# Kernel tuning notes

Measured on AMD Instinct MI355X. Metric: run time of the kernel, lower is better.

## Reference

```python
import jax, jax.numpy as jnp
import numpy as np

FS = 160        # frame shift (samples per frame)
MU = 255.0      # mu-law constant for 256 levels
EMPH = 0.97     # de-emphasis coefficient


def _conv_tanh(x, w, b):
    # Conv1dKeepLength (non-causal, same-length) + tanh. x: (B,L,Cin), w: (K,Cin,Cout)
    K = w.shape[0]
    pad_le = (K - 1) // 2
    pad_ri = (K - 1) - pad_le
    xp = jnp.pad(x, ((0, 0), (pad_le, pad_ri), (0, 0)))
    L = x.shape[1]
    y = b
    for k in range(K):  # tiny fixed kernel loop (K=3)
        y = y + xp[:, k:k + L, :] @ w[k]
    return jnp.tanh(y)


def _forward(features, conv1_w, conv1_b, conv2_w, conv2_b,
             fr_fc1_w, fr_fc1_b, fr_fc2_w, fr_fc2_b,
             gru_wi, gru_wh, gru_bi, gru_bh, out_w, out_b):
    # ---- FrameRateNet: conv-tanh x2 + MLP -> conditioning (B,F,128) ----
    c = _conv_tanh(features, conv1_w, conv1_b)
    c = _conv_tanh(c, conv2_w, conv2_b)
    c = jnp.tanh(c @ fr_fc1_w + fr_fc1_b)
    cond = jnp.tanh(c @ fr_fc2_w + fr_fc2_b)
    # upsample frame-rate conditioning to sample rate: (B, T=F*FS, 128)
    cond_up = jnp.repeat(cond, FS, axis=1)
    B, T, _ = cond_up.shape
    H = gru_wh.shape[1]
    dt = features.dtype

    def step(carry, cond_t):
        h, prev = carry                       # h:(B,H)  prev:(B,1) last emitted sample
        x = jnp.concatenate([prev, cond_t], axis=-1)   # (B, 1+128)
        gi = x @ gru_wi.T + gru_bi            # (B, 3H)
        gh = h @ gru_wh.T + gru_bh
        i_r, i_z, i_n = jnp.split(gi, 3, axis=-1)
        h_r, h_z, h_n = jnp.split(gh, 3, axis=-1)
        r = jax.nn.sigmoid(i_r + h_r)
        z = jax.nn.sigmoid(i_z + h_z)
        n = jnp.tanh(i_n + r * h_n)
        h_new = (1.0 - z) * n + z * h
        logits = h_new @ out_w + out_b        # (B, 256) mu-law categorical logits
        idx = jnp.argmax(logits, axis=-1)     # greedy sampling (deterministic baseline)
        v = (idx.astype(dt) + 0.5) / 128.0 - 1.0           # (-1,1)
        sample = jnp.sign(v) * (jnp.power(1.0 + MU, jnp.abs(v)) - 1.0) / MU
        return (h_new, sample[:, None]), (logits, sample)

    cond_seq = jnp.swapaxes(cond_up, 0, 1)    # (T,B,128)
    init = (jnp.zeros((B, H), dt), jnp.zeros((B, 1), dt))
    _, (logits, samples) = jax.lax.scan(step, init, cond_seq)
    logits = jnp.swapaxes(logits, 0, 1)       # (B,T,256)
    samples = jnp.swapaxes(samples, 0, 1)     # (B,T)

    # ---- de-emphasis IIR: y[t] = s[t] + 0.97*y[t-1] ----
    def de_step(y_prev, s_t):
        y = s_t + EMPH * y_prev
        return y, y
    _, wav = jax.lax.scan(de_step, jnp.zeros((B,), dt), samples.T)
    wav = wav.T[..., None]                    # (B,T,1)
    return wav, logits


def setup_inputs() -> dict:
    key = jax.random.key(0)
    ks = jax.random.split(key, 16)
    B, F, D = 8, 64, 20
    s = 0.05
    return {
        "features": jax.random.normal(ks[0], (B, F, D), jnp.float32),
        "conv1_w": jax.random.normal(ks[1], (3, D, 128), jnp.float32) * s,
        "conv1_b": jnp.zeros((128,), jnp.float32),
        "conv2_w": jax.random.normal(ks[2], (3, 128, 128), jnp.float32) * s,
        "conv2_b": jnp.zeros((128,), jnp.float32),
        "fr_fc1_w": jax.random.normal(ks[3], (128, 128), jnp.float32) * s,
        "fr_fc1_b": jnp.zeros((128,), jnp.float32),
        "fr_fc2_w": jax.random.normal(ks[4], (128, 128), jnp.float32) * s,
        "fr_fc2_b": jnp.zeros((128,), jnp.float32),
        "gru_wi": jax.random.normal(ks[5], (768, 129), jnp.float32) * s,
        "gru_wh": jax.random.normal(ks[6], (768, 256), jnp.float32) * s,
        "gru_bi": jnp.zeros((768,), jnp.float32),
        "gru_bh": jnp.zeros((768,), jnp.float32),
        "out_w": jax.random.normal(ks[7], (256, 256), jnp.float32) * s,
        "out_b": jnp.zeros((256,), jnp.float32),
    }


def reference(features, conv1_w, conv1_b, conv2_w, conv2_b,
              fr_fc1_w, fr_fc1_b, fr_fc2_w, fr_fc2_b,
              gru_wi, gru_wh, gru_bi, gru_bh, out_w, out_b):
    return _forward(features, conv1_w, conv1_b, conv2_w, conv2_b,
                    fr_fc1_w, fr_fc1_b, fr_fc2_w, fr_fc2_b,
                    gru_wi, gru_wh, gru_bi, gru_bh, out_w, out_b)
```

## Files before the change

### kernel.cpp

```cpp
#include <hip/hip_runtime.h>
#include <cmath>


#define NB 8
#define NF 64
#define ND 20
#define NH 256
#define NG 768
#define FS 160
#define NT (NF * FS)
#define NSLOT 768

#define AGENT __HIP_MEMORY_SCOPE_AGENT
#define HLAY(c) ((((c) >> 4) * 20) + ((c) & 15))

typedef float v2f __attribute__((ext_vector_type(2)));

#define PKFMA(acc, w, h) \
    asm("v_pk_fma_f32 %0, %1, %2, %0" : "+v"(acc) : "v"(w), "v"(h))
#define PKFMA_BLO(acc, w, h) \
    asm("v_pk_fma_f32 %0, %1, %2, %0 op_sel:[0,0,0] op_sel_hi:[1,0,1]" \
        : "+v"(acc) : "v"(w), "v"(h))
#define PKFMA_BHI(acc, w, h) \
    asm("v_pk_fma_f32 %0, %1, %2, %0 op_sel:[0,1,0] op_sel_hi:[1,1,1]" \
        : "+v"(acc) : "v"(w), "v"(h))

#define DPP0(x, ctrl) \
    __int_as_float(__builtin_amdgcn_update_dpp( \
        0, __float_as_int(x), (ctrl), 0xf, 0xf, true))
#define DPPOLD(x, ctrl, oldv) \
    __int_as_float(__builtin_amdgcn_update_dpp( \
        __float_as_int(oldv), __float_as_int(x), (ctrl), 0xf, 0xf, false))

static __device__ __forceinline__ float fexp2(float x) {
    float r; asm("v_exp_f32 %0, %1" : "=v"(r) : "v"(x)); return r;
}
static __device__ __forceinline__ float frcp(float x) {
    float r; asm("v_rcp_f32 %0, %1" : "=v"(r) : "v"(x)); return r;
}
#define LOG2E  1.4426950408889634f
#define LOG2E2 2.8853900817779268f
static __device__ __forceinline__ float fsigmoid(float x) {
    return frcp(1.f + fexp2(-x * LOG2E));
}
static __device__ __forceinline__ float ftanh(float x) {
    return 1.f - 2.f * frcp(fexp2(x * LOG2E2) + 1.f);
}

#define BAR() do { \
    __builtin_amdgcn_sched_barrier(0); \
    asm volatile("s_waitcnt lgkmcnt(0)" ::: "memory"); \
    __builtin_amdgcn_s_barrier(); \
    __builtin_amdgcn_sched_barrier(0); } while (0)

__global__ __launch_bounds__(128) void frn_kernel(
    const float* __restrict__ feat,
    const float* __restrict__ w1,
    const float* __restrict__ b1,
    const float* __restrict__ w2,
    const float* __restrict__ b2,
    const float* __restrict__ fw1,
    const float* __restrict__ fb1,
    const float* __restrict__ fw2,
    const float* __restrict__ fb2,
    const float* __restrict__ wi,
    const float* __restrict__ bi,
    float* __restrict__ gic)
{
    const int bf = blockIdx.x;
    const int b = bf >> 6;
    const int f = bf & 63;
    const int o = threadIdx.x;

    __shared__ float sfeat[5][ND];
    __shared__ float sc1[3][128];
    __shared__ float sc2[128];
    __shared__ float sc3[128];
    __shared__ float scond[128];

    for (int i = o; i < 5 * ND; i += 128) {
        int ff = f - 2 + i / ND;
        int c = i % ND;
        sfeat[i / ND][c] = (ff >= 0 && ff < NF) ? feat[((size_t)b * NF + ff) * ND + c] : 0.f;
    }
    __syncthreads();

    for (int df = 0; df < 3; ++df) {
        int fp = f - 1 + df;
        if (fp >= 0 && fp < NF) {
            float acc = b1[o];
            for (int k = 0; k < 3; ++k)
                for (int c = 0; c < ND; ++c)
                    acc += sfeat[df + k][c] * w1[(k * ND + c) * 128 + o];
            sc1[df][o] = tanhf(acc);
        } else {
            sc1[df][o] = 0.f;
        }
    }
    __syncthreads();

    {
        float acc = b2[o];
        for (int k = 0; k < 3; ++k)
            for (int c = 0; c < 128; ++c)
                acc += sc1[k][c] * w2[(k * 128 + c) * 128 + o];
        sc2[o] = tanhf(acc);
    }
    __syncthreads();
    {
        float acc = fb1[o];
        for (int c = 0; c < 128; ++c) acc += sc2[c] * fw1[c * 128 + o];
        sc3[o] = tanhf(acc);
    }
    __syncthreads();
    {
        float acc = fb2[o];
        for (int c = 0; c < 128; ++c) acc += sc3[c] * fw2[c * 128 + o];
        scond[o] = tanhf(acc);
    }
    __syncthreads();

    for (int r = 0; r < 6; ++r) {
        int j = o + 128 * r;
        float acc = bi[j];
        const float* wr = wi + (size_t)j * 129 + 1;
        for (int c = 0; c < 128; ++c) acc += scond[c] * wr[c];
        gic[(size_t)bf * NG + j] = acc;
    }
}

__global__ __launch_bounds__(512, 2) void ar_kernel(
    const float* __restrict__ gic,
    const float* __restrict__ wh,
    const float* __restrict__ ow,
    const float* __restrict__ wi,
    const float* __restrict__ bh,
    const float* __restrict__ ob,
    float* __restrict__ wav_out,
    float* __restrict__ logits_out,
    unsigned long long* __restrict__ hxp)
{
    const int bid = blockIdx.x;
    const int b = bid & 7;
    const int j = bid >> 3;
    const int t = threadIdx.x;
    const int qq = t >> 4;
    const int ss = t & 15;
    const int og = t >> 3;
    const int c8 = t & 7;

    __shared__ __align__(16) float hsp[16 * 20];
    __shared__ __align__(16) float pl[8][260];
    __shared__ float sgi[NG];
    __shared__ float candv[4];
    __shared__ int   candi[4];

    v2f WH0[8], WH1[8], WH2[8];
    {
        const v2f* wb2 = (const v2f*)wh;
        size_t q0 = (size_t)(32 * j + qq) * 128 + ss * 8;
        #pragma unroll
        for (int i = 0; i < 8; ++i) {
            WH0[i] = wb2[q0 + i];
            WH1[i] = wb2[q0 + 256 * 128 + i];
            WH2[i] = wb2[q0 + 512 * 128 + i];
        }
    }
    v2f OWa[32], OWb[32];
    {
        const v2f* op2 = (const v2f*)ow;
        #pragma unroll
        for (int i = 0; i < 32; ++i) {
            OWa[i] = op2[(size_t)(c8 * 32 + i) * 128 + og * 2];
            OWb[i] = op2[(size_t)(c8 * 32 + i) * 128 + og * 2 + 1];
        }
    }

    float bh_r = 0, bh_z = 0, bh_n = 0, wi_r = 0, wi_z = 0, wi_n = 0, ob_o = 0;
    if (t < NH) {
        bh_r = bh[t]; bh_z = bh[t + 256]; bh_n = bh[t + 512];
        wi_r = wi[(size_t)t * 129];
        wi_z = wi[(size_t)(t + 256) * 129];
        wi_n = wi[(size_t)(t + 512) * 129];
        ob_o = ob[t];
        hsp[HLAY(t)] = 0.f;
    }
    float prev = 0.f, yacc = 0.f;
    __syncthreads();

    const float* gf = gic + (size_t)b * NF * NG;
    float* lob = logits_out + (size_t)b * NT * NH;
    float* wob = wav_out + (size_t)b * NT;
    unsigned long long* hxb = hxp + (size_t)b * 2 * NSLOT;
    int fcnt = 0;

    for (int st = 0; st <= NT; ++st) {
        if (st < NT && fcnt == 0) {
            for (int i = t; i < NG; i += 512) sgi[i] = gf[i];
        }

        {
            const float4* h4 = (const float4*)hsp;
            float4 ha0 = h4[ss * 5 + 0];
            float4 ha1 = h4[ss * 5 + 1];
            float4 ha2 = h4[ss * 5 + 2];
            float4 ha3 = h4[ss * 5 + 3];
            float4 hb0 = h4[(c8 * 2) * 5 + 0];
            float4 hb1 = h4[(c8 * 2) * 5 + 1];
            float4 hb2 = h4[(c8 * 2) * 5 + 2];
            float4 hb3 = h4[(c8 * 2) * 5 + 3];
            float4 hb4 = h4[(c8 * 2 + 1) * 5 + 0];
            float4 hb5 = h4[(c8 * 2 + 1) * 5 + 1];
            float4 hb6 = h4[(c8 * 2 + 1) * 5 + 2];
            float4 hb7 = h4[(c8 * 2 + 1) * 5 + 3];

            v2f s0 = {0.f, 0.f}, s1 = {0.f, 0.f}, s2 = {0.f, 0.f};
            {
                v2f lo, hi;
                lo.x = ha0.x; lo.y = ha0.y; hi.x = ha0.z; hi.y = ha0.w;
                PKFMA(s0, WH0[0], lo); PKFMA(s0, WH0[1], hi);
                PKFMA(s1, WH1[0], lo); PKFMA(s1, WH1[1], hi);
                PKFMA(s2, WH2[0], lo); PKFMA(s2, WH2[1], hi);
                lo.x = ha1.x; lo.y = ha1.y; hi.x = ha1.z; hi.y = ha1.w;
                PKFMA(s0, WH0[2], lo); PKFMA(s0, WH0[3], hi);
                PKFMA(s1, WH1[2], lo); PKFMA(s1, WH1[3], hi);
                PKFMA(s2, WH2[2], lo); PKFMA(s2, WH2[3], hi);
                lo.x = ha2.x; lo.y = ha2.y; hi.x = ha2.z; hi.y = ha2.w;
                PKFMA(s0, WH0[4], lo); PKFMA(s0, WH0[5], hi);
                PKFMA(s1, WH1[4], lo); PKFMA(s1, WH1[5], hi);
                PKFMA(s2, WH2[4], lo); PKFMA(s2, WH2[5], hi);
                lo.x = ha3.x; lo.y = ha3.y; hi.x = ha3.z; hi.y = ha3.w;
                PKFMA(s0, WH0[6], lo); PKFMA(s0, WH0[7], hi);
                PKFMA(s1, WH1[6], lo); PKFMA(s1, WH1[7], hi);
                PKFMA(s2, WH2[6], lo); PKFMA(s2, WH2[7], hi);
            }
            float a0 = s0.x + s0.y, a1 = s1.x + s1.y, a2 = s2.x + s2.y;
            a0 += DPP0(a0, 0x111); a1 += DPP0(a1, 0x111); a2 += DPP0(a2, 0x111);
            a0 += DPP0(a0, 0x112); a1 += DPP0(a1, 0x112); a2 += DPP0(a2, 0x112);
            a0 += DPP0(a0, 0x114); a1 += DPP0(a1, 0x114); a2 += DPP0(a2, 0x114);
            a0 += DPP0(a0, 0x118); a1 += DPP0(a1, 0x118); a2 += DPP0(a2, 0x118);
            if (st < NT && ss == 15) {
                unsigned long long tg = (unsigned long long)(unsigned)(st + 1) << 32;
                size_t base = (size_t)(st & 1) * NSLOT + 32 * j + qq;
                (void)__hip_atomic_exchange(&hxb[base],
                    tg | (unsigned long long)__float_as_uint(a0),
                    __ATOMIC_RELAXED, AGENT);
                (void)__hip_atomic_exchange(&hxb[base + 256],
                    tg | (unsigned long long)__float_as_uint(a1),
                    __ATOMIC_RELAXED, AGENT);
                (void)__hip_atomic_exchange(&hxb[base + 512],
                    tg | (unsigned long long)__float_as_uint(a2),
                    __ATOMIC_RELAXED, AGENT);
            }

            v2f acc01 = {0.f, 0.f}, acc23 = {0.f, 0.f};
            {
                v2f h01, h23;
                #define A2STEP(hv, ia) \
                    h01.x = hv.x; h01.y = hv.y; h23.x = hv.z; h23.y = hv.w; \
                    PKFMA_BLO(acc01, OWa[4*(ia)+0], h01); \
                    PKFMA_BLO(acc23, OWb[4*(ia)+0], h01); \
                    PKFMA_BHI(acc01, OWa[4*(ia)+1], h01); \
                    PKFMA_BHI(acc23, OWb[4*(ia)+1], h01); \
                    PKFMA_BLO(acc01, OWa[4*(ia)+2], h23); \
                    PKFMA_BLO(acc23, OWb[4*(ia)+2], h23); \
                    PKFMA_BHI(acc01, OWa[4*(ia)+3], h23); \
                    PKFMA_BHI(acc23, OWb[4*(ia)+3], h23);
                A2STEP(hb0, 0) A2STEP(hb1, 1) A2STEP(hb2, 2) A2STEP(hb3, 3)
                A2STEP(hb4, 4) A2STEP(hb5, 5) A2STEP(hb6, 6) A2STEP(hb7, 7)
                #undef A2STEP
            }
            float4 outv;
            outv.x = acc01.x; outv.y = acc01.y;
            outv.z = acc23.x; outv.w = acc23.y;
            *(float4*)&pl[c8][og * 4] = outv;
        }
        BAR();

        unsigned long long g0 = 0, g1 = 0, g2 = 0;
        if (st < NT && t < NH) {
            unsigned long long* hb = hxb + (size_t)(st & 1) * NSLOT;
            g0 = __hip_atomic_load(&hb[t], __ATOMIC_RELAXED, AGENT);
            g1 = __hip_atomic_load(&hb[NH + t], __ATOMIC_RELAXED, AGENT);
            g2 = __hip_atomic_load(&hb[2 * NH + t], __ATOMIC_RELAXED, AGENT);
        }

        float lgs = 0.f;
        if (st > 0 && t < NH) {
            float lg = ob_o;
            #pragma unroll
            for (int c = 0; c < 8; ++c) lg += pl[c][t];
            lgs = lg;
            const float NINF = -__builtin_inff();
            float m = lg;
            m = fmaxf(m, DPPOLD(m, 0x111, NINF));
            m = fmaxf(m, DPPOLD(m, 0x112, NINF));
            m = fmaxf(m, DPPOLD(m, 0x114, NINF));
            m = fmaxf(m, DPPOLD(m, 0x118, NINF));
            m = fmaxf(m, DPPOLD(m, 0x142, NINF));
            m = fmaxf(m, DPPOLD(m, 0x143, NINF));
            float wmax = __int_as_float(
                __builtin_amdgcn_readlane(__float_as_int(m), 63));
            unsigned long long msk = __ballot(lg == wmax);
            int lidx = __ffsll((unsigned long long)msk) - 1;
            if ((t & 63) == 0) {
                candv[t >> 6] = wmax;
                candi[t >> 6] = (t & ~63) + lidx;
            }
        }
        BAR();

        if (st > 0) {
            float mv = candv[0]; int mi = candi[0];
            #pragma unroll
            for (int w = 1; w < 4; ++w) {
                float ov = candv[w]; int oi = candi[w];
                if (ov > mv || (ov == mv && oi < mi)) { mv = ov; mi = oi; }
            }
            float v = ((float)mi + 0.5f) * (1.f / 128.f) - 1.f;
            float av = fabsf(v);
            float mag = (fexp2(8.f * av) - 1.f) * (1.f / 255.f);
            float smp = (v >= 0.f) ? mag : -mag;
            prev = smp;
            yacc = smp + 0.97f * yacc;
        }

        if (st < NT && t < NH) {
            const unsigned tag = (unsigned)(st + 1);
            unsigned long long* hb = hxb + (size_t)(st & 1) * NSLOT;
            asm volatile("s_waitcnt vmcnt(0)"
                         : "+v"(g0), "+v"(g1), "+v"(g2) :: "memory");
            __builtin_amdgcn_sched_barrier(0);
            int spin = 0;
            while (((unsigned)(g0 >> 32) != tag) |
                   ((unsigned)(g1 >> 32) != tag) |
                   ((unsigned)(g2 >> 32) != tag)) {
                ++spin;
                if ((spin & 3) == 3) __builtin_amdgcn_s_sleep(1);
                if ((unsigned)(g0 >> 32) != tag)
                    g0 = __hip_atomic_load(&hb[t], __ATOMIC_RELAXED, AGENT);
                if ((unsigned)(g1 >> 32) != tag)
                    g1 = __hip_atomic_load(&hb[NH + t], __ATOMIC_RELAXED, AGENT);
                if ((unsigned)(g2 >> 32) != tag)
                    g2 = __hip_atomic_load(&hb[2 * NH + t], __ATOMIC_RELAXED, AGENT);
            }
            float ghr = __uint_as_float((unsigned)g0);
            float ghz = __uint_as_float((unsigned)g1);
            float ghn = __uint_as_float((unsigned)g2);
            float sr = sgi[t]          + wi_r * prev + bh_r + ghr;
            float sz = sgi[t + NH]     + wi_z * prev + bh_z + ghz;
            float ni = sgi[t + 2 * NH] + wi_n * prev;
            float nh = bh_n + ghn;
            float r = fsigmoid(sr);
            float z = fsigmoid(sz);
            float n = ftanh(ni + r * nh);
            int hl = HLAY(t);
            hsp[hl] = (1.f - z) * n + z * hsp[hl];
        }

        if (st > 0) {
            if (t < NH && (t >> 5) == j) lob[(size_t)(st - 1) * NH + t] = lgs;
            if (j == 0 && t == 0)        wob[st - 1] = yacc;
        }
        BAR();

        if (st < NT) {
            if (++fcnt == FS) { fcnt = 0; gf += NG; }
        }
    }
}

extern "C" void kernel_launch(void* const* d_in, const int* in_sizes, int n_in,
                              void* d_out, int out_size, void* d_ws, size_t ws_size,
                              hipStream_t stream) {
    (void)in_sizes; (void)n_in; (void)out_size; (void)ws_size;

    const float* feat = (const float*)d_in[0];
    const float* c1w  = (const float*)d_in[1];
    const float* c1b  = (const float*)d_in[2];
    const float* c2w  = (const float*)d_in[3];
    const float* c2b  = (const float*)d_in[4];
    const float* f1w  = (const float*)d_in[5];
    const float* f1b  = (const float*)d_in[6];
    const float* f2w  = (const float*)d_in[7];
    const float* f2b  = (const float*)d_in[8];
    const float* gwi  = (const float*)d_in[9];
    const float* gwh  = (const float*)d_in[10];
    const float* gbi  = (const float*)d_in[11];
    const float* gbh  = (const float*)d_in[12];
    const float* outw = (const float*)d_in[13];
    const float* outb = (const float*)d_in[14];

    char* ws = (char*)d_ws;
    float* gic = (float*)ws;
    unsigned long long* hxp = (unsigned long long*)(ws + 1572864);

    float* wav    = (float*)d_out;
    float* logits = (float*)d_out + NB * NT;

    frn_kernel<<<dim3(NB * NF), dim3(128), 0, stream>>>(
        feat, c1w, c1b, c2w, c2b, f1w, f1b, f2w, f2b, gwi, gbi, gic);
    ar_kernel<<<dim3(64), dim3(512), 0, stream>>>(
        gic, gwh, outw, gwi, gbh, outb, wav, logits, hxp);
}
```

Before: 18.42 ms.

## Replace per-step workgroup barriers with LDS counter arrive/poll synchronization

Swaps the three s_barrier calls per autoregressive step for per-wave atomic arrive counters in LDS that consumers poll with acquire loads. Only waves 0-3 do the logits reduction, argmax and GRU update; waves 4-7 skip that phase and sleep-poll until the new hidden state is ready. The argmax candidates are packed into one 64-bit value, and the FMA chains are split across twice as many accumulators for more instruction-level parallelism. The goal is to cut barrier stalls on the serial critical path. In exchange it adds spin-polling, which competes for issue slots, and depends on subtle memory-ordering behaviour.

```diff
diff --git a/kernel.cpp b/kernel.cpp
--- a/kernel.cpp
+++ b/kernel.cpp
@@ -11,7 +11,8 @@
 #define NT (NF * FS)
 #define NSLOT 768
 
-#define AGENT __HIP_MEMORY_SCOPE_AGENT
+#define AGENT  __HIP_MEMORY_SCOPE_AGENT
+#define WGSC   __HIP_MEMORY_SCOPE_WORKGROUP
 #define HLAY(c) ((((c) >> 4) * 20) + ((c) & 15))
 
 typedef float v2f __attribute__((ext_vector_type(2)));
@@ -47,10 +48,19 @@
     return 1.f - 2.f * frcp(fexp2(x * LOG2E2) + 1.f);
 }
 
-#define BAR() do { \
+#define ARRIVE(cntp) do { \
     __builtin_amdgcn_sched_barrier(0); \
     asm volatile("s_waitcnt lgkmcnt(0)" ::: "memory"); \
-    __builtin_amdgcn_s_barrier(); \
+    if ((t & 63) == 0) \
+        (void)__hip_atomic_fetch_add((cntp), 1u, __ATOMIC_RELAXED, WGSC); \
+    __builtin_amdgcn_sched_barrier(0); } while (0)
+#define POLL_GE(cntp, tgt) do { \
+    while ((int)__hip_atomic_load((cntp), __ATOMIC_ACQUIRE, WGSC) \
+           - (int)(tgt) < 0) {} \
+    __builtin_amdgcn_sched_barrier(0); } while (0)
+#define POLL_GE_SLEEP(cntp, tgt) do { \
+    while ((int)__hip_atomic_load((cntp), __ATOMIC_ACQUIRE, WGSC) \
+           - (int)(tgt) < 0) { __builtin_amdgcn_s_sleep(1); } \
     __builtin_amdgcn_sched_barrier(0); } while (0)
 
 __global__ __launch_bounds__(128) void frn_kernel(
@@ -144,6 +154,7 @@
     const int b = bid & 7;
     const int j = bid >> 3;
     const int t = threadIdx.x;
+    const int wv = t >> 6;
     const int qq = t >> 4;
     const int ss = t & 15;
     const int og = t >> 3;
@@ -152,8 +163,8 @@
     __shared__ __align__(16) float hsp[16 * 20];
     __shared__ __align__(16) float pl[8][260];
     __shared__ float sgi[NG];
-    __shared__ float candv[4];
-    __shared__ int   candi[4];
+    __shared__ unsigned long long candk[4];
+    __shared__ unsigned cnt_pl, cnt_cand, cnt_hsp;
 
     v2f WH0[8], WH1[8], WH2[8];
     {
@@ -185,6 +196,7 @@
         ob_o = ob[t];
         hsp[HLAY(t)] = 0.f;
     }
+    if (t == 0) { cnt_pl = 0; cnt_cand = 0; cnt_hsp = 0; }
     float prev = 0.f, yacc = 0.f;
     __syncthreads();
 
@@ -195,6 +207,11 @@
     int fcnt = 0;
 
     for (int st = 0; st <= NT; ++st) {
+        if (st > 0) {
+            if (wv >= 4) { POLL_GE_SLEEP(&cnt_hsp, 4u * (unsigned)st); }
+            else         { POLL_GE(&cnt_hsp, 4u * (unsigned)st); }
+        }
+
         if (st < NT && fcnt == 0) {
             for (int i = t; i < NG; i += 512) sgi[i] = gf[i];
         }
@@ -214,27 +231,30 @@
             float4 hb6 = h4[(c8 * 2 + 1) * 5 + 2];
             float4 hb7 = h4[(c8 * 2 + 1) * 5 + 3];
 
-            v2f s0 = {0.f, 0.f}, s1 = {0.f, 0.f}, s2 = {0.f, 0.f};
+            v2f s0a = {0,0}, s0b = {0,0}, s1a = {0,0},
+                s1b = {0,0}, s2a = {0,0}, s2b = {0,0};
             {
                 v2f lo, hi;
                 lo.x = ha0.x; lo.y = ha0.y; hi.x = ha0.z; hi.y = ha0.w;
-                PKFMA(s0, WH0[0], lo); PKFMA(s0, WH0[1], hi);
-                PKFMA(s1, WH1[0], lo); PKFMA(s1, WH1[1], hi);
-                PKFMA(s2, WH2[0], lo); PKFMA(s2, WH2[1], hi);
+                PKFMA(s0a, WH0[0], lo); PKFMA(s0b, WH0[1], hi);
+                PKFMA(s1a, WH1[0], lo); PKFMA(s1b, WH1[1], hi);
+                PKFMA(s2a, WH2[0], lo); PKFMA(s2b, WH2[1], hi);
                 lo.x = ha1.x; lo.y = ha1.y; hi.x = ha1.z; hi.y = ha1.w;
-                PKFMA(s0, WH0[2], lo); PKFMA(s0, WH0[3], hi);
-                PKFMA(s1, WH1[2], lo); PKFMA(s1, WH1[3], hi);
-                PKFMA(s2, WH2[2], lo); PKFMA(s2, WH2[3], hi);
+                PKFMA(s0a, WH0[2], lo); PKFMA(s0b, WH0[3], hi);
+                PKFMA(s1a, WH1[2], lo); PKFMA(s1b, WH1[3], hi);
+                PKFMA(s2a, WH2[2], lo); PKFMA(s2b, WH2[3], hi);
                 lo.x = ha2.x; lo.y = ha2.y; hi.x = ha2.z; hi.y = ha2.w;
-                PKFMA(s0, WH0[4], lo); PKFMA(s0, WH0[5], hi);
-                PKFMA(s1, WH1[4], lo); PKFMA(s1, WH1[5], hi);
-                PKFMA(s2, WH2[4], lo); PKFMA(s2, WH2[5], hi);
+                PKFMA(s0a, WH0[4], lo); PKFMA(s0b, WH0[5], hi);
+                PKFMA(s1a, WH1[4], lo); PKFMA(s1b, WH1[5], hi);
+                PKFMA(s2a, WH2[4], lo); PKFMA(s2b, WH2[5], hi);
                 lo.x = ha3.x; lo.y = ha3.y; hi.x = ha3.z; hi.y = ha3.w;
-                PKFMA(s0, WH0[6], lo); PKFMA(s0, WH0[7], hi);
-                PKFMA(s1, WH1[6], lo); PKFMA(s1, WH1[7], hi);
-                PKFMA(s2, WH2[6], lo); PKFMA(s2, WH2[7], hi);
-            }
-            float a0 = s0.x + s0.y, a1 = s1.x + s1.y, a2 = s2.x + s2.y;
+                PKFMA(s0a, WH0[6], lo); PKFMA(s0b, WH0[7], hi);
+                PKFMA(s1a, WH1[6], lo); PKFMA(s1b, WH1[7], hi);
+                PKFMA(s2a, WH2[6], lo); PKFMA(s2b, WH2[7], hi);
+            }
+            float a0 = (s0a.x + s0a.y) + (s0b.x + s0b.y);
+            float a1 = (s1a.x + s1a.y) + (s1b.x + s1b.y);
+            float a2 = (s2a.x + s2a.y) + (s2b.x + s2b.y);
             a0 += DPP0(a0, 0x111); a1 += DPP0(a1, 0x111); a2 += DPP0(a2, 0x111);
             a0 += DPP0(a0, 0x112); a1 += DPP0(a1, 0x112); a2 += DPP0(a2, 0x112);
             a0 += DPP0(a0, 0x114); a1 += DPP0(a1, 0x114); a2 += DPP0(a2, 0x114);
@@ -253,116 +273,133 @@
                     __ATOMIC_RELAXED, AGENT);
             }
 
-            v2f acc01 = {0.f, 0.f}, acc23 = {0.f, 0.f};
+            v2f p01a = {0,0}, p01b = {0,0}, p23a = {0,0}, p23b = {0,0};
             {
                 v2f h01, h23;
-                #define A2STEP(hv, ia) \
+                #define A2STEP(hv, ia, A01, A23) \
                     h01.x = hv.x; h01.y = hv.y; h23.x = hv.z; h23.y = hv.w; \
-                    PKFMA_BLO(acc01, OWa[4*(ia)+0], h01); \
-                    PKFMA_BLO(acc23, OWb[4*(ia)+0], h01); \
-                    PKFMA_BHI(acc01, OWa[4*(ia)+1], h01); \
-                    PKFMA_BHI(acc23, OWb[4*(ia)+1], h01); \
-                    PKFMA_BLO(acc01, OWa[4*(ia)+2], h23); \
-                    PKFMA_BLO(acc23, OWb[4*(ia)+2], h23); \
-                    PKFMA_BHI(acc01, OWa[4*(ia)+3], h23); \
-                    PKFMA_BHI(acc23, OWb[4*(ia)+3], h23);
-                A2STEP(hb0, 0) A2STEP(hb1, 1) A2STEP(hb2, 2) A2STEP(hb3, 3)
-                A2STEP(hb4, 4) A2STEP(hb5, 5) A2STEP(hb6, 6) A2STEP(hb7, 7)
+                    PKFMA_BLO(A01, OWa[4*(ia)+0], h01); \
+                    PKFMA_BLO(A23, OWb[4*(ia)+0], h01); \
+                    PKFMA_BHI(A01, OWa[4*(ia)+1], h01); \
+                    PKFMA_BHI(A23, OWb[4*(ia)+1], h01); \
+                    PKFMA_BLO(A01, OWa[4*(ia)+2], h23); \
+                    PKFMA_BLO(A23, OWb[4*(ia)+2], h23); \
+                    PKFMA_BHI(A01, OWa[4*(ia)+3], h23); \
+                    PKFMA_BHI(A23, OWb[4*(ia)+3], h23);
+                A2STEP(hb0, 0, p01a, p23a) A2STEP(hb1, 1, p01a, p23a)
+                A2STEP(hb2, 2, p01a, p23a) A2STEP(hb3, 3, p01a, p23a)
+                A2STEP(hb4, 4, p01b, p23b) A2STEP(hb5, 5, p01b, p23b)
+                A2STEP(hb6, 6, p01b, p23b) A2STEP(hb7, 7, p01b, p23b)
                 #undef A2STEP
             }
             float4 outv;
-            outv.x = acc01.x; outv.y = acc01.y;
-            outv.z = acc23.x; outv.w = acc23.y;
+            outv.x = p01a.x + p01b.x; outv.y = p01a.y + p01b.y;
+            outv.z = p23a.x + p23b.x; outv.w = p23a.y + p23b.y;
             *(float4*)&pl[c8][og * 4] = outv;
         }
-        BAR();
-
-        unsigned long long g0 = 0, g1 = 0, g2 = 0;
-        if (st < NT && t < NH) {
-            unsigned long long* hb = hxb + (size_t)(st & 1) * NSLOT;
-            g0 = __hip_atomic_load(&hb[t], __ATOMIC_RELAXED, AGENT);
-            g1 = __hip_atomic_load(&hb[NH + t], __ATOMIC_RELAXED, AGENT);
-            g2 = __hip_atomic_load(&hb[2 * NH + t], __ATOMIC_RELAXED, AGENT);
-        }
-
-        float lgs = 0.f;
-        if (st > 0 && t < NH) {
-            float lg = ob_o;
-            #pragma unroll
-            for (int c = 0; c < 8; ++c) lg += pl[c][t];
-            lgs = lg;
-            const float NINF = -__builtin_inff();
-            float m = lg;
-            m = fmaxf(m, DPPOLD(m, 0x111, NINF));
-            m = fmaxf(m, DPPOLD(m, 0x112, NINF));
-            m = fmaxf(m, DPPOLD(m, 0x114, NINF));
-            m = fmaxf(m, DPPOLD(m, 0x118, NINF));
-            m = fmaxf(m, DPPOLD(m, 0x142, NINF));
-            m = fmaxf(m, DPPOLD(m, 0x143, NINF));
-            float wmax = __int_as_float(
-                __builtin_amdgcn_readlane(__float_as_int(m), 63));
-            unsigned long long msk = __ballot(lg == wmax);
-            int lidx = __ffsll((unsigned long long)msk) - 1;
-            if ((t & 63) == 0) {
-                candv[t >> 6] = wmax;
-                candi[t >> 6] = (t & ~63) + lidx;
-            }
-        }
-        BAR();
-
-        if (st > 0) {
-            float mv = candv[0]; int mi = candi[0];
-            #pragma unroll
-            for (int w = 1; w < 4; ++w) {
-                float ov = candv[w]; int oi = candi[w];
+        ARRIVE(&cnt_pl);
+
+        if (wv < 4) {
+            POLL_GE(&cnt_pl, 8u * (unsigned)(st + 1));
+
+            unsigned long long g0 = 0, g1 = 0, g2 = 0;
+            if (st < NT) {
+                unsigned long long* hb = hxb + (size_t)(st & 1) * NSLOT;
+                g0 = __hip_atomic_load(&hb[t], __ATOMIC_RELAXED, AGENT);
+                g1 = __hip_atomic_load(&hb[NH + t], __ATOMIC_RELAXED, AGENT);
+                g2 = __hip_atomic_load(&hb[2 * NH + t], __ATOMIC_RELAXED, AGENT);
+            }
+
+            float lgs = 0.f;
+            if (st > 0) {
+                float q0 = pl[0][t] + pl[1][t];
+                float q1 = pl[2][t] + pl[3][t];
+                float q2 = pl[4][t] + pl[5][t];
+                float q3 = pl[6][t] + pl[7][t];
+                float lg = ob_o + ((q0 + q1) + (q2 + q3));
+                lgs = lg;
+                const float NINF = -__builtin_inff();
+                float m = lg;
+                m = fmaxf(m, DPPOLD(m, 0x111, NINF));
+                m = fmaxf(m, DPPOLD(m, 0x112, NINF));
+                m = fmaxf(m, DPPOLD(m, 0x114, NINF));
+                m = fmaxf(m, DPPOLD(m, 0x118, NINF));
+                m = fmaxf(m, DPPOLD(m, 0x142, NINF));
+                m = fmaxf(m, DPPOLD(m, 0x143, NINF));
+                float wmax = __int_as_float(
+                    __builtin_amdgcn_readlane(__float_as_int(m), 63));
+                unsigned long long msk = __ballot(lg == wmax);
+                int lidx = __ffsll((unsigned long long)msk) - 1;
+                if ((t & 63) == 0) {
+                    unsigned long long pkk =
+                        ((unsigned long long)(unsigned)((wv << 6) + lidx) << 32)
+                        | (unsigned long long)__float_as_uint(wmax);
+                    __hip_atomic_store(&candk[wv], pkk, __ATOMIC_RELAXED, WGSC);
+                }
+                ARRIVE(&cnt_cand);
+            }
+
+            if (st > 0) {
+                POLL_GE(&cnt_cand, 4u * (unsigned)st);
+                unsigned long long c0 = __hip_atomic_load(&candk[0], __ATOMIC_RELAXED, WGSC);
+                unsigned long long c1 = __hip_atomic_load(&candk[1], __ATOMIC_RELAXED, WGSC);
+                unsigned long long c2 = __hip_atomic_load(&candk[2], __ATOMIC_RELAXED, WGSC);
+                unsigned long long c3 = __hip_atomic_load(&candk[3], __ATOMIC_RELAXED, WGSC);
+                float mv = __uint_as_float((unsigned)c0); int mi = (int)(c0 >> 32);
+                float ov; int oi;
+                ov = __uint_as_float((unsigned)c1); oi = (int)(c1 >> 32);
                 if (ov > mv || (ov == mv && oi < mi)) { mv = ov; mi = oi; }
-            }
-            float v = ((float)mi + 0.5f) * (1.f / 128.f) - 1.f;
-            float av = fabsf(v);
-            float mag = (fexp2(8.f * av) - 1.f) * (1.f / 255.f);
-            float smp = (v >= 0.f) ? mag : -mag;
-            prev = smp;
-            yacc = smp + 0.97f * yacc;
-        }
-
-        if (st < NT && t < NH) {
-            const unsigned tag = (unsigned)(st + 1);
-            unsigned long long* hb = hxb + (size_t)(st & 1) * NSLOT;
-            asm volatile("s_waitcnt vmcnt(0)"
-                         : "+v"(g0), "+v"(g1), "+v"(g2) :: "memory");
-            __builtin_amdgcn_sched_barrier(0);
-            int spin = 0;
-            while (((unsigned)(g0 >> 32) != tag) |
-                   ((unsigned)(g1 >> 32) != tag) |
-                   ((unsigned)(g2 >> 32) != tag)) {
-                ++spin;
-                if ((spin & 3) == 3) __builtin_amdgcn_s_sleep(1);
-                if ((unsigned)(g0 >> 32) != tag)
-                    g0 = __hip_atomic_load(&hb[t], __ATOMIC_RELAXED, AGENT);
-                if ((unsigned)(g1 >> 32) != tag)
-                    g1 = __hip_atomic_load(&hb[NH + t], __ATOMIC_RELAXED, AGENT);
-                if ((unsigned)(g2 >> 32) != tag)
-                    g2 = __hip_atomic_load(&hb[2 * NH + t], __ATOMIC_RELAXED, AGENT);
-            }
-            float ghr = __uint_as_float((unsigned)g0);
-            float ghz = __uint_as_float((unsigned)g1);
-            float ghn = __uint_as_float((unsigned)g2);
-            float sr = sgi[t]          + wi_r * prev + bh_r + ghr;
-            float sz = sgi[t + NH]     + wi_z * prev + bh_z + ghz;
-            float ni = sgi[t + 2 * NH] + wi_n * prev;
-            float nh = bh_n + ghn;
-            float r = fsigmoid(sr);
-            float z = fsigmoid(sz);
-            float n = ftanh(ni + r * nh);
-            int hl = HLAY(t);
-            hsp[hl] = (1.f - z) * n + z * hsp[hl];
-        }
-
-        if (st > 0) {
-            if (t < NH && (t >> 5) == j) lob[(size_t)(st - 1) * NH + t] = lgs;
-            if (j == 0 && t == 0)        wob[st - 1] = yacc;
-        }
-        BAR();
+                ov = __uint_as_float((unsigned)c2); oi = (int)(c2 >> 32);
+                if (ov > mv || (ov == mv && oi < mi)) { mv = ov; mi = oi; }
+                ov = __uint_as_float((unsigned)c3); oi = (int)(c3 >> 32);
+                if (ov > mv || (ov == mv && oi < mi)) { mv = ov; mi = oi; }
+                float v = ((float)mi + 0.5f) * (1.f / 128.f) - 1.f;
+                float av = fabsf(v);
+                float mag = (fexp2(8.f * av) - 1.f) * (1.f / 255.f);
+                float smp = (v >= 0.f) ? mag : -mag;
+                prev = smp;
+                yacc = smp + 0.97f * yacc;
+            }
+
+            if (st < NT) {
+                const unsigned tag = (unsigned)(st + 1);
+                unsigned long long* hb = hxb + (size_t)(st & 1) * NSLOT;
+                asm volatile("s_waitcnt vmcnt(0)"
+                             : "+v"(g0), "+v"(g1), "+v"(g2) :: "memory");
+                __builtin_amdgcn_sched_barrier(0);
+                int spin = 0;
+                while (((unsigned)(g0 >> 32) != tag) |
+                       ((unsigned)(g1 >> 32) != tag) |
+                       ((unsigned)(g2 >> 32) != tag)) {
+                    ++spin;
+                    if ((spin & 3) == 3) __builtin_amdgcn_s_sleep(1);
+                    if ((unsigned)(g0 >> 32) != tag)
+                        g0 = __hip_atomic_load(&hb[t], __ATOMIC_RELAXED, AGENT);
+                    if ((unsigned)(g1 >> 32) != tag)
+                        g1 = __hip_atomic_load(&hb[NH + t], __ATOMIC_RELAXED, AGENT);
+                    if ((unsigned)(g2 >> 32) != tag)
+                        g2 = __hip_atomic_load(&hb[2 * NH + t], __ATOMIC_RELAXED, AGENT);
+                }
+                float ghr = __uint_as_float((unsigned)g0);
+                float ghz = __uint_as_float((unsigned)g1);
+                float ghn = __uint_as_float((unsigned)g2);
+                float sr = sgi[t]          + wi_r * prev + bh_r + ghr;
+                float sz = sgi[t + NH]     + wi_z * prev + bh_z + ghz;
+                float ni = sgi[t + 2 * NH] + wi_n * prev;
+                float nh = bh_n + ghn;
+                float r = fsigmoid(sr);
+                float z = fsigmoid(sz);
+                float n = ftanh(ni + r * nh);
+                int hl = HLAY(t);
+                hsp[hl] = (1.f - z) * n + z * hsp[hl];
+                ARRIVE(&cnt_hsp);
+            }
+
+            if (st > 0) {
+                if ((t >> 5) == j) lob[(size_t)(st - 1) * NH + t] = lgs;
+                if (j == 0 && t == 0) wob[st - 1] = yacc;
+            }
+        }
 
         if (st < NT) {
             if (++fcnt == FS) { fcnt = 0; gf += NG; }
```

Result: slower. 24.67 ms (+33.9%).
